# Optimization experiments

Measured on AMD Instinct MI355X. Metric: run time of the kernel, lower is better.

Reference implementation:

```python
import jax, jax.numpy as jnp
import numpy as np

NH = 12      # attention heads
EPS = 1e-5   # torch nn.LayerNorm default


def _ln(x, g, b):
    m = jnp.mean(x, axis=-1, keepdims=True)
    v = jnp.var(x, axis=-1, keepdims=True)
    return (x - m) * jax.lax.rsqrt(v + EPS) * g + b


def _rel_table(table, n):
    # q_size == k_size == n, table length == 2n-1 -> pure gather, no interpolation
    idx = jnp.arange(n)[:, None] - jnp.arange(n)[None, :] + (n - 1)
    return table[idx]  # (n, n, head_dim)


def _attn2d(x, qkv_w, qkv_b, proj_w, proj_b, rel_h, rel_w):
    B, H, W, C = x.shape
    hd = C // NH
    scale = hd ** -0.5
    N = H * W
    qkv = x.reshape(B, N, C) @ qkv_w + qkv_b                    # (B, N, 3C)
    qkv = qkv.reshape(B, N, 3, NH, hd).transpose(2, 0, 3, 1, 4).reshape(3, B * NH, N, hd)
    q, k, v = qkv[0], qkv[1], qkv[2]
    attn = jnp.einsum('bnd,bmd->bnm', q * scale, k)             # (B*NH, N, N)
    Rh = _rel_table(rel_h, H)
    Rw = _rel_table(rel_w, W)
    rq = q.reshape(B * NH, H, W, hd)                            # unscaled q, as in torch
    bias_h = jnp.einsum('bhwc,hkc->bhwk', rq, Rh)
    bias_w = jnp.einsum('bhwc,wkc->bhwk', rq, Rw)
    attn = (attn.reshape(B * NH, H, W, H, W)
            + bias_h[:, :, :, :, None]
            + bias_w[:, :, :, None, :]).reshape(B * NH, N, N)
    attn = jax.nn.softmax(attn, axis=-1)
    out = (attn @ v).reshape(B, NH, H, W, hd).transpose(0, 2, 3, 1, 4).reshape(B, H, W, C)
    return out @ proj_w + proj_b


def _win_part(x, ws):
    B, H, W, C = x.shape
    ph = (ws - H % ws) % ws
    pw = (ws - W % ws) % ws
    x = jnp.pad(x, ((0, 0), (0, ph), (0, pw), (0, 0)))
    Hp, Wp = H + ph, W + pw
    x = x.reshape(B, Hp // ws, ws, Wp // ws, ws, C).transpose(0, 1, 3, 2, 4, 5)
    return x.reshape(-1, ws, ws, C), (Hp, Wp)


def _win_unpart(wins, ws, pad_hw, hw):
    Hp, Wp = pad_hw
    H, W = hw
    B = wins.shape[0] // (Hp * Wp // ws // ws)
    x = wins.reshape(B, Hp // ws, Wp // ws, ws, ws, -1).transpose(0, 1, 3, 2, 4, 5)
    x = x.reshape(B, Hp, Wp, -1)
    return x[:, :H, :W, :]


def _block(x, ws, ln1g, ln1b, qkvw, qkvb, projw, projb, relh, relw,
           ln2g, ln2b, mw1, mb1, mw2, mb2):
    shortcut = x
    x = _ln(x, ln1g, ln1b)
    if ws > 0:
        H, W = x.shape[1], x.shape[2]
        x, pad_hw = _win_part(x, ws)
    x = _attn2d(x, qkvw, qkvb, projw, projb, relh, relw)
    if ws > 0:
        x = _win_unpart(x, ws, pad_hw, (H, W))
    x = shortcut + x
    h = _ln(x, ln2g, ln2b)
    h = jax.nn.gelu(h @ mw1 + mb1, approximate=False) @ mw2 + mb2
    return x + h


def setup_inputs() -> dict:
    key = jax.random.key(0)
    def rnd(i, shape, s=0.02):
        return jax.random.normal(jax.random.fold_in(key, i), shape, jnp.float32) * s
    C, M, HD = 768, 3072, 64
    d = {
        'x': rnd(0, (1, 3, 1024, 1024), 1.0),
        'patch_w': rnd(1, (16, 16, 3, C)),
        'patch_b': rnd(2, (C,)),
        'pos_embed': rnd(3, (1, 64, 64, C)),
    }
    i = 4
    for s, L in (('1', 27), ('2', 127)):
        for name, shape in (('ln1g', (C,)), ('ln1b', (C,)), ('qkvw', (C, 3 * C)),
                            ('qkvb', (3 * C,)), ('projw', (C, C)), ('projb', (C,)),
                            ('relh', (L, HD)), ('relw', (L, HD)),
                            ('ln2g', (C,)), ('ln2b', (C,)),
                            ('mw1', (C, M)), ('mb1', (M,)), ('mw2', (M, C)), ('mb2', (C,))):
            d[name + s] = rnd(i, shape)
            i += 1
    for s in ('1', '2'):
        d['ln1g' + s] = d['ln1g' + s] + 1.0
        d['ln2g' + s] = d['ln2g' + s] + 1.0
    return d


def reference(x, patch_w, patch_b, pos_embed,
              ln1g1, ln1b1, qkvw1, qkvb1, projw1, projb1, relh1, relw1,
              ln2g1, ln2b1, mw11, mb11, mw21, mb21,
              ln1g2, ln1b2, qkvw2, qkvb2, projw2, projb2, relh2, relw2,
              ln2g2, ln2b2, mw12, mb12, mw22, mb22):
    # patch embed: 16x16 stride-16 conv, output NHWC (B, 64, 64, 768)
    feat = jax.lax.conv_general_dilated(
        x, patch_w, window_strides=(16, 16), padding='VALID',
        dimension_numbers=('NCHW', 'HWIO', 'NHWC'))
    feat = feat + patch_b + pos_embed
    feat = _block(feat, 14, ln1g1, ln1b1, qkvw1, qkvb1, projw1, projb1,
                  relh1, relw1, ln2g1, ln2b1, mw11, mb11, mw21, mb21)
    feat = _block(feat, 0, ln1g2, ln1b2, qkvw2, qkvb2, projw2, projb2,
                  relh2, relw2, ln2g2, ln2b2, mw12, mb12, mw22, mb22)
    return feat
```

## Files before the change

kernel.cpp:

```cpp
#include <hip/hip_runtime.h>


using u16 = unsigned short;
using u32 = unsigned int;
using short8  = __attribute__((ext_vector_type(8))) short;
using floatx4 = __attribute__((ext_vector_type(4))) float;

__device__ __forceinline__ float bfu2f(u16 u) { return __builtin_bit_cast(float, (u32)u << 16); }
__device__ __forceinline__ u16   f2bfu(float f) {
  u32 u = __builtin_bit_cast(u32, f);
  return (u16)((u + 0x7fffu + ((u >> 16) & 1u)) >> 16);
}
#define DIV14(x) (((x) * 4682) >> 16)
#define WAIT_VM0()   __builtin_amdgcn_s_waitcnt(0x3f70)
#define WAIT_LGKM0() __builtin_amdgcn_s_waitcnt(0xc07f)

__device__ __forceinline__ void gld_lds16(const u16* g, u16* l) {
  __builtin_amdgcn_global_load_lds(
      (const __attribute__((address_space(1))) u32*)g,
      (__attribute__((address_space(3))) u32*)l, 16, 0, 0);
}

__global__ __launch_bounds__(256) void detect_k(const u16* __restrict__ x, int* __restrict__ flag)
{
  __shared__ int tot;
  if (threadIdx.x == 0) tot = 0;
  __syncthreads();
  int cnt = 0;
  for (int i = threadIdx.x; i < 4096; i += 256) {
    int e = (x[2 * i] >> 7) & 0xFF;
    cnt += (e >= 100 && e <= 134) ? 1 : 0;
  }
  atomicAdd(&tot, cnt);
  __syncthreads();
  if (threadIdx.x == 0) *flag = (tot >= 2458) ? 1 : 0;
}

struct CvtEnt { const void* src; int n; int dstoff; };
struct CvtArgs { CvtEnt e[24]; int cnt; };

__global__ __launch_bounds__(256) void tobf_multi_k(CvtArgs a, u16* __restrict__ dst,
                                                    const int* __restrict__ flag)
{
  int gid = blockIdx.x * 256 + threadIdx.x;
  bool isbf = (*flag != 0);
  for (int t = 0; t < a.cnt; ++t)
    if (gid < a.e[t].n)
      dst[a.e[t].dstoff + gid] = isbf ? ((const u16*)a.e[t].src)[gid]
                                      : f2bfu(((const float*)a.e[t].src)[gid]);
}

__global__ __launch_bounds__(256) void tobf4_k(const void* __restrict__ src, u16* __restrict__ dst,
                                               int n4, const int* __restrict__ flag)
{
  int i = blockIdx.x * 256 + threadIdx.x;
  if (i >= n4) return;
  ushort4 o;
  if (*flag) o = ((const ushort4*)src)[i];
  else {
    float4 f = ((const float4*)src)[i];
    o.x = f2bfu(f.x); o.y = f2bfu(f.y); o.z = f2bfu(f.z); o.w = f2bfu(f.w);
  }
  ((ushort4*)dst)[i] = o;
}

__global__ __launch_bounds__(256) void tobfT_k(const void* __restrict__ src, u16* __restrict__ dst,
                                               int K, int N, const int* __restrict__ flag)
{
  __shared__ u16 t[64][65];
  const int n0 = blockIdx.x * 64, k0 = blockIdx.y * 64;
  const int r = threadIdx.x >> 2, c = (threadIdx.x & 3) * 16;
  if (*flag) {
    const u16* s = (const u16*)src + (size_t)(k0 + r) * N + n0 + c;
    union { uint4 v[2]; u16 e[16]; } u;
    u.v[0] = *(const uint4*)s; u.v[1] = *(const uint4*)(s + 8);
    #pragma unroll
    for (int j = 0; j < 16; ++j) t[c + j][r] = u.e[j];
  } else {
    const float* s = (const float*)src + (size_t)(k0 + r) * N + n0 + c;
    #pragma unroll
    for (int j = 0; j < 16; ++j) t[c + j][r] = f2bfu(s[j]);
  }
  __syncthreads();
  union { uint4 v[2]; u16 e[16]; } o;
  #pragma unroll
  for (int j = 0; j < 16; ++j) o.e[j] = t[r][c + j];
  u16* d = dst + (size_t)(n0 + r) * K + k0 + c;
  *(uint4*)d = o.v[0]; *(uint4*)(d + 8) = o.v[1];
}

__global__ __launch_bounds__(256) void im2col_k(const void* __restrict__ xv, u16* __restrict__ a,
                                                const int* __restrict__ flag)
{
  int t = blockIdx.x, tid = threadIdx.x;
  int py = t >> 6, px = t & 63;
  int ky = tid >> 4, kx = tid & 15;
  size_t src = (size_t)(py * 16 + ky) * 1024 + px * 16 + kx;
  u16 v0, v1, v2;
  if (*flag) {
    const u16* x = (const u16*)xv;
    v0 = x[src]; v1 = x[src + 1048576]; v2 = x[src + 2097152];
  } else {
    const float* x = (const float*)xv;
    v0 = f2bfu(x[src]); v1 = f2bfu(x[src + 1048576]); v2 = f2bfu(x[src + 2097152]);
  }
  size_t dst = (size_t)t * 768 + tid * 3;
  a[dst] = v0; a[dst + 1] = v1; a[dst + 2] = v2;
}

__global__ __launch_bounds__(256) void ln_k(const float* __restrict__ x,
                                            const u16* __restrict__ g,
                                            const u16* __restrict__ b,
                                            u16* __restrict__ y)
{
  const int t = blockIdx.x, tid = threadIdx.x;
  const float* xp = x + (size_t)t * 768;
  float v0 = xp[tid], v1 = xp[tid + 256], v2 = xp[tid + 512];
  float s = v0 + v1 + v2;
  float q = v0 * v0 + v1 * v1 + v2 * v2;
  #pragma unroll
  for (int off = 32; off; off >>= 1) { s += __shfl_xor(s, off); q += __shfl_xor(q, off); }
  __shared__ float red[8];
  int wid = tid >> 6, lane = tid & 63;
  if (lane == 0) { red[wid] = s; red[4 + wid] = q; }
  __syncthreads();
  s = red[0] + red[1] + red[2] + red[3];
  q = red[4] + red[5] + red[6] + red[7];
  float mean = s * (1.f / 768.f);
  float var  = q * (1.f / 768.f) - mean * mean;
  float rstd = rsqrtf(var + 1e-5f);
  u16* yp = y + (size_t)t * 768;
  yp[tid]       = f2bfu((v0 - mean) * rstd * bfu2f(g[tid])       + bfu2f(b[tid]));
  yp[tid + 256] = f2bfu((v1 - mean) * rstd * bfu2f(g[tid + 256]) + bfu2f(b[tid + 256]));
  yp[tid + 512] = f2bfu((v2 - mean) * rstd * bfu2f(g[tid + 512]) + bfu2f(b[tid + 512]));
}

__global__ __launch_bounds__(256) void win_part_k(const u16* __restrict__ ln, u16* __restrict__ w)
{
  int vid = blockIdx.x * 256 + threadIdx.x;
  if (vid >= 470400) return;
  size_t idx = (size_t)vid * 8;
  int c = (int)(idx % 768);
  int r = (int)(idx / 768);
  int win = r / 196, tok = r - win * 196;
  int gy = (win / 5) * 14 + tok / 14;
  int gx = (win % 5) * 14 + tok % 14;
  uint4 v = make_uint4(0, 0, 0, 0);
  if (gy < 64 && gx < 64)
    v = *(const uint4*)(ln + ((size_t)(gy * 64 + gx) * 768 + c));
  *(uint4*)(w + idx) = v;
}

enum { MODE_FEAT = 0, MODE_QKV = 1, MODE_RES = 2, MODE_GELU = 3, MODE_OUT = 4 };

template<int BN>
__global__ __launch_bounds__(256) void mgemm_k(
    const u16* __restrict__ A, const u16* __restrict__ Bt, const u16* __restrict__ bias,
    int M, int N, int K, int mode,
    float* __restrict__ outf, u16* __restrict__ outb,
    const float* __restrict__ res, const u16* __restrict__ pos,
    u16* __restrict__ qb, u16* __restrict__ kb, u16* __restrict__ vt, int TW,
    const int* __restrict__ flagp)
{
  constexpr int NWN = BN / 64, NWM = 4 / NWN;
  constexpr int WTM = 128 / NWM;
  constexpr int MS = WTM / 16, NS = 4;
  __shared__ __align__(16) u16 As[2][128 * 32];
  __shared__ __align__(16) u16 Bs[2][BN * 32];
  const int tid = threadIdx.x;
  const int wid = tid >> 6, lane = tid & 63;
  const int l15 = lane & 15, quad = lane >> 4;
  const int wm = wid / NWN, wn = wid % NWN;
  const int m0 = blockIdx.y * 128, n0 = blockIdx.x * BN;

  floatx4 acc[MS][NS];
  #pragma unroll
  for (int i = 0; i < MS; ++i)
    #pragma unroll
    for (int j = 0; j < NS; ++j) acc[i][j] = (floatx4){0.f, 0.f, 0.f, 0.f};

  const int sr = lane >> 2, sc = (lane & 3) * 8;
  const u16* ag0 = A + (size_t)min(m0 + wid * 32 + sr,      M - 1) * K + sc;
  const u16* ag1 = A + (size_t)min(m0 + wid * 32 + 16 + sr, M - 1) * K + sc;
  const u16 *bg0 = nullptr, *bg1 = nullptr;
  if constexpr (BN == 128) {
    bg0 = Bt + (size_t)(n0 + wid * 32 + sr) * K + sc;
    bg1 = Bt + (size_t)(n0 + wid * 32 + 16 + sr) * K + sc;
  } else {
    bg0 = Bt + (size_t)(n0 + wid * 16 + sr) * K + sc;
  }

  auto issue = [&](int buf, int k0) {
    gld_lds16(ag0 + k0, &As[buf][(wid * 32) * 32]);
    gld_lds16(ag1 + k0, &As[buf][(wid * 32 + 16) * 32]);
    if constexpr (BN == 128) {
      gld_lds16(bg0 + k0, &Bs[buf][(wid * 32) * 32]);
      gld_lds16(bg1 + k0, &Bs[buf][(wid * 32 + 16) * 32]);
    } else {
      gld_lds16(bg0 + k0, &Bs[buf][(wid * 16) * 32]);
    }
  };

  issue(0, 0);
  int bufi = 0;
  for (int k0 = 0; k0 < K; k0 += 32, bufi ^= 1) {
    WAIT_VM0();
    __syncthreads();
    if (k0 + 32 < K) issue(bufi ^ 1, k0 + 32);
    short8 af[MS], bf[NS];
    #pragma unroll
    for (int ms = 0; ms < MS; ++ms)
      af[ms] = *(const short8*)&As[bufi][(wm * WTM + ms * 16 + l15) * 32 + quad * 8];
    #pragma unroll
    for (int ns = 0; ns < NS; ++ns)
      bf[ns] = *(const short8*)&Bs[bufi][(wn * 64 + ns * 16 + l15) * 32 + quad * 8];
    #pragma unroll
    for (int ms = 0; ms < MS; ++ms)
      #pragma unroll
      for (int ns = 0; ns < NS; ++ns)
        acc[ms][ns] = __builtin_amdgcn_mfma_f32_16x16x32_bf16(af[ms], bf[ns], acc[ms][ns], 0, 0, 0);
  }

  const bool outbf = (mode == MODE_OUT) ? (*flagp != 0) : false;
  #pragma unroll
  for (int ms = 0; ms < MS; ++ms) {
    const int gmb = m0 + wm * WTM + ms * 16 + quad * 4;
    #pragma unroll
    for (int ns = 0; ns < NS; ++ns) {
      const int gn = n0 + wn * 64 + ns * 16 + l15;
      const float bb = bfu2f(bias[gn]);
      if (mode == MODE_QKV) {
        const int s = gn / 768, nn = gn - s * 768, h = nn >> 6, d = nn & 63;
        #pragma unroll
        for (int r = 0; r < 4; ++r) {
          int gm = gmb + r; if (gm >= M) continue;
          float v = acc[ms][ns][r] + bb;
          int b = gm / TW, tok = gm - b * TW;
          size_t bh = (size_t)(b * 12 + h);
          if (s == 0)      qb[(bh * TW + tok) * 64 + d] = f2bfu(v);
          else if (s == 1) kb[(bh * TW + tok) * 64 + d] = f2bfu(v);
          else             vt[(bh * 64 + d) * TW + tok] = f2bfu(v);
        }
      } else {
        #pragma unroll
        for (int r = 0; r < 4; ++r) {
          int gm = gmb + r; if (gm >= M) continue;
          size_t o = (size_t)gm * N + gn;
          float v = acc[ms][ns][r] + bb;
          if (mode == MODE_FEAT)      outf[o] = v + bfu2f(pos[o]);
          else if (mode == MODE_RES)  outf[o] = v + res[o];
          else if (mode == MODE_GELU) outb[o] = f2bfu(0.5f * v * (1.f + erff(v * 0.70710678f)));
          else {
            float ov = v + res[o];
            if (outbf) outb[o] = f2bfu(ov);
            else       outf[o] = ov;
          }
        }
      }
    }
  }
}

template<int NT, int TD, bool WIN>
__global__ __launch_bounds__(256) void flash_k(
    const u16* __restrict__ qb, const u16* __restrict__ kb, const u16* __restrict__ vt,
    const u16* __restrict__ relh, const u16* __restrict__ relw,
    u16* __restrict__ outb)
{
  constexpr int NTAB = 2 * TD - 1;
  constexpr int KT = (NT + 63) >> 6;
  constexpr float L2E = 1.4426950408889634f;
  constexpr float SC2 = 0.125f * L2E;
  constexpr int RQ  = 0;
  constexpr int RK0 = 4096;
  constexpr int RK1 = WIN ? 4096 : 8192;
  constexpr int RV0 = WIN ? 8192 : 12288;
  constexpr int RV1 = WIN ? 8192 : 16384;
  constexpr int RG  = WIN ? 12288 : 20480;
  constexpr int GWWIN = RG + 64 * 34;
  constexpr int TOT = WIN ? (GWWIN + 64 * 34) : (RG + 64 * 66);
  __shared__ __align__(16) u16 lds[TOT];

  const int tid = threadIdx.x, wid = tid >> 6, lane = tid & 63;
  const int l15 = lane & 15, quad = lane >> 4;
  const int qt = blockIdx.x, bh = blockIdx.y;
  const int q0 = qt * 64;
  const size_t kvbase = (size_t)bh * NT * 64;
  const size_t vbase  = (size_t)bh * 64 * NT;

  auto swb = [](int row, int blk) { return row * 64 + (((blk ^ row) & 7) << 3); };

  {
    const int r = tid >> 2, cb = (tid & 3) * 2;
    const int tok = min(q0 + r, NT - 1);
    const uint4* p = (const uint4*)(qb + kvbase + (size_t)tok * 64 + cb * 8);
    *(uint4*)&lds[RQ + swb(r, cb)]     = p[0];
    *(uint4*)&lds[RQ + swb(r, cb + 1)] = p[1];
  }
  __syncthreads();
  short8 qf[2];
  qf[0] = *(const short8*)&lds[RQ + swb(wid * 16 + l15, quad)];
  qf[1] = *(const short8*)&lds[RQ + swb(wid * 16 + l15, 4 + quad)];
  WAIT_LGKM0();

  auto stageRB = [&](const u16* tab, int rowoff, int maxrow) {
    const int r = tid >> 2, cb = (tid & 3) * 2;
    const int tr = min(rowoff + r, maxrow);
    const uint4* p = (const uint4*)(tab + (size_t)tr * 64 + cb * 8);
    *(uint4*)&lds[RV0 + swb(r, cb)]     = p[0];
    *(uint4*)&lds[RV0 + swb(r, cb + 1)] = p[1];
  };
  auto gpass = [&](int gbase, int gstride, int ncols) {
    for (int ns = 0; ns < ncols / 16; ++ns) {
      floatx4 g = (floatx4){0.f, 0.f, 0.f, 0.f};
      #pragma unroll
      for (int ks = 0; ks < 2; ++ks) {
        short8 b = *(const short8*)&lds[RV0 + swb(ns * 16 + l15, ks * 4 + quad)];
        g = __builtin_amdgcn_mfma_f32_16x16x32_bf16(qf[ks], b, g, 0, 0, 0);
      }
      #pragma unroll
      for (int r = 0; r < 4; ++r)
        lds[gbase + (wid * 16 + quad * 4 + r) * gstride + ns * 16 + l15] = f2bfu(g[r] * L2E);
    }
  };

  float gwv[4][4];
  if constexpr (!WIN) {
    stageRB(relh, qt, NTAB - 1);  __syncthreads();
    gpass(RG, 66, 64);
    __syncthreads();
    stageRB(relw, 0, NTAB - 1);   __syncthreads();
    gpass(RK0, 66, 64);
    #pragma unroll
    for (int r = 0; r < 4; ++r) {
      const int tr = wid * 16 + quad * 4 + r;
      #pragma unroll
      for (int ns = 0; ns < 4; ++ns) {
        const int iw = tr - (ns * 16 + l15) + 63;
        if (iw < 64) gwv[ns][r] = bfu2f(lds[RK0 + tr * 66 + iw]);
      }
    }
    WAIT_LGKM0();
    __syncthreads();
    stageRB(relw, 64, NTAB - 1);  __syncthreads();
    gpass(RK0, 66, 64);
    #pragma unroll
    for (int r = 0; r < 4; ++r) {
      const int tr = wid * 16 + quad * 4 + r;
      #pragma unroll
      for (int ns = 0; ns < 4; ++ns) {
        const int iw = tr - (ns * 16 + l15) + 63;
        if (iw >= 64) gwv[ns][r] = bfu2f(lds[RK0 + tr * 66 + iw - 64]);
      }
    }
    WAIT_LGKM0();
  } else {
    stageRB(relh, 0, NTAB - 1);  __syncthreads();
    gpass(RG, 34, 32);
    __syncthreads();
    stageRB(relw, 0, NTAB - 1);  __syncthreads();
    gpass(GWWIN, 34, 32);
  }

  const int srow = lane >> 3;
  const int scol = (((lane & 7) ^ srow) & 7) << 3;
  const u16* kg = kb + kvbase + (size_t)(wid * 16 + srow) * 64 + scol;
  const u16* vg = vt + vbase  + (size_t)(wid * 16 + srow) * NT + scol;
  auto issue = [&](int buf, int kt2) {
    const u16* k0 = kg + (size_t)kt2 * 4096;
    const u16* v0 = vg + kt2 * 64;
    u16* kd = &lds[(buf ? RK1 : RK0) + wid * 16 * 64];
    u16* vd = &lds[(buf ? RV1 : RV0) + wid * 16 * 64];
    gld_lds16(k0,           kd);
    gld_lds16(k0 + 512,     kd + 512);
    gld_lds16(v0,           vd);
    gld_lds16(v0 + 8 * NT,  vd + 512);
  };

  float mI[4], lI[4];
  floatx4 Oacc[4];
  #pragma unroll
  for (int r = 0; r < 4; ++r) { mI[r] = -3e38f; lI[r] = 0.f; }
  #pragma unroll
  for (int d = 0; d < 4; ++d) Oacc[d] = (floatx4){0.f, 0.f, 0.f, 0.f};

  if constexpr (!WIN) { __syncthreads(); issue(0, 0); }

  for (int kt = 0; kt < KT; ++kt) {
    int RKb, RVb;
    if constexpr (!WIN) {
      WAIT_VM0();
      __syncthreads();
      if (kt + 1 < KT) issue((kt + 1) & 1, kt + 1);
      RKb = (kt & 1) ? RK1 : RK0;
      RVb = (kt & 1) ? RV1 : RV0;
    } else {
      __syncthreads();
      {
        const int r = tid >> 2, cb = (tid & 3) * 2;
        const int key = min(kt * 64 + r, NT - 1);
        const uint4* p = (const uint4*)(kb + kvbase + (size_t)key * 64 + cb * 8);
        *(uint4*)&lds[RK0 + swb(r, cb)]     = p[0];
        *(uint4*)&lds[RK0 + swb(r, cb + 1)] = p[1];
      }
      {
        const int d = tid >> 2, c = (tid & 3) << 4;
        #pragma unroll
        for (int j = 0; j < 16; ++j) {
          int key = min(kt * 64 + c + j, NT - 1);
          const int col = c + j;
          lds[RV0 + d * 64 + (((((col >> 3)) ^ d) & 7) << 3) + (col & 7)] =
              vt[vbase + (size_t)d * NT + key];
        }
      }
      __syncthreads();
      RKb = RK0; RVb = RV0;
    }

    floatx4 sacc[4];
    #pragma unroll
    for (int ns = 0; ns < 4; ++ns) sacc[ns] = (floatx4){0.f, 0.f, 0.f, 0.f};
    #pragma unroll
    for (int ks = 0; ks < 2; ++ks)
      #pragma unroll
      for (int ns = 0; ns < 4; ++ns) {
        short8 b = *(const short8*)&lds[RKb + swb(ns * 16 + l15, ks * 4 + quad)];
        sacc[ns] = __builtin_amdgcn_mfma_f32_16x16x32_bf16(qf[ks], b, sacc[ns], 0, 0, 0);
      }

    float sv[4][4];
    #pragma unroll
    for (int r = 0; r < 4; ++r) {
      if constexpr (!WIN) {
        #pragma unroll
        for (int ns = 0; ns < 4; ++ns)
          sv[ns][r] = fmaf(SC2, sacc[ns][r], gwv[ns][r]);
      } else {
        const int tr = wid * 16 + quad * 4 + r;
        const int tok = q0 + tr;
        const int qy = DIV14(tok), qx = tok - 14 * qy;
        #pragma unroll
        for (int ns = 0; ns < 4; ++ns) {
          const int j = kt * 64 + ns * 16 + l15;
          const int ky = DIV14(j), kx = j - 14 * ky;
          int ih = qy - ky + 13; ih = max(0, min(ih, 31));
          int iw = qx - kx + 13; iw = max(0, min(iw, 31));
          float s = SC2 * sacc[ns][r] + bfu2f(lds[RG + tr * 34 + ih])
                                      + bfu2f(lds[GWWIN + tr * 34 + iw]);
          sv[ns][r] = (j < NT) ? s : -1e30f;
        }
      }
    }

    #pragma unroll
    for (int r = 0; r < 4; ++r) {
      const int tr = wid * 16 + quad * 4 + r;
      float rm = fmaxf(fmaxf(sv[0][r], sv[1][r]), fmaxf(sv[2][r], sv[3][r]));
      #pragma unroll
      for (int off = 1; off < 16; off <<= 1) rm = fmaxf(rm, __shfl_xor(rm, off));
      float ghv = 0.f;
      if constexpr (!WIN) ghv = bfu2f(lds[RG + tr * 66 + (63 - kt)]);
      const float mt = rm + ghv;
      const float mn = fmaxf(mI[r], mt);
      const float al = __builtin_amdgcn_exp2f(mI[r] - mn);
      mI[r] = mn;
      const float t = mn - ghv;
      float rs = 0.f;
      #pragma unroll
      for (int ns = 0; ns < 4; ++ns) {
        float p = __builtin_amdgcn_exp2f(sv[ns][r] - t);
        rs += p;
        const int col = ns * 16 + l15;
        lds[RQ + tr * 64 + ((((col >> 3) ^ tr) & 7) << 3) + (col & 7)] = f2bfu(p);
      }
      #pragma unroll
      for (int off = 1; off < 16; off <<= 1) rs += __shfl_xor(rs, off);
      lI[r] = lI[r] * al + rs;
      #pragma unroll
      for (int d = 0; d < 4; ++d) Oacc[d][r] *= al;
    }

    #pragma unroll
    for (int ks = 0; ks < 2; ++ks) {
      short8 a = *(const short8*)&lds[RQ + swb(wid * 16 + l15, ks * 4 + quad)];
      #pragma unroll
      for (int d = 0; d < 4; ++d) {
        short8 b = *(const short8*)&lds[RVb + swb(d * 16 + l15, ks * 4 + quad)];
        Oacc[d] = __builtin_amdgcn_mfma_f32_16x16x32_bf16(a, b, Oacc[d], 0, 0, 0);
      }
    }
  }

  #pragma unroll
  for (int r = 0; r < 4; ++r) {
    const int tr = wid * 16 + quad * 4 + r;
    const float rinv = 1.f / lI[r];
    const int tok = q0 + tr;
    if constexpr (WIN) {
      if (tok >= NT) continue;
      const int win = bh / 12, h = bh - win * 12;
      const int ty = DIV14(tok), tx = tok - 14 * ty;
      const int gy = (win / 5) * 14 + ty, gx = (win % 5) * 14 + tx;
      if (gy >= 64 || gx >= 64) continue;
      u16* op = outb + (size_t)(gy * 64 + gx) * 768 + h * 64;
      #pragma unroll
      for (int d = 0; d < 4; ++d) op[d * 16 + l15] = f2bfu(Oacc[d][r] * rinv);
    } else {
      u16* op = outb + (size_t)tok * 768 + bh * 64;
      #pragma unroll
      for (int d = 0; d < 4; ++d) op[d * 16 + l15] = f2bfu(Oacc[d][r] * rinv);
    }
  }
}

extern "C" void kernel_launch(void* const* d_in, const int* in_sizes, int n_in,
                              void* d_out, int out_size, void* d_ws, size_t ws_size,
                              hipStream_t stream)
{
  const void* x      = d_in[0];
  const void* patchw = d_in[1];
  const void* patchb = d_in[2];
  const void* pos    = d_in[3];
  const void *ln1g1 = d_in[4],  *ln1b1 = d_in[5];
  const void *qkvw1 = d_in[6],  *qkvb1 = d_in[7];
  const void *projw1= d_in[8],  *projb1= d_in[9];
  const void *relh1 = d_in[10], *relw1 = d_in[11];
  const void *ln2g1 = d_in[12], *ln2b1 = d_in[13];
  const void *mw11  = d_in[14], *mb11  = d_in[15];
  const void *mw21  = d_in[16], *mb21  = d_in[17];
  const void *ln1g2 = d_in[18], *ln1b2 = d_in[19];
  const void *qkvw2 = d_in[20], *qkvb2 = d_in[21];
  const void *projw2= d_in[22], *projb2= d_in[23];
  const void *relh2 = d_in[24], *relw2 = d_in[25];
  const void *ln2g2 = d_in[26], *ln2b2 = d_in[27];
  const void *mw12  = d_in[28], *mb12  = d_in[29];
  const void *mw22  = d_in[30], *mb22  = d_in[31];

  char* w = (char*)d_ws;
  int*   FLAG = (int*)w;  w += 64;
  float* R0 = (float*)w;  w += 12582912;
  float* R1 = (float*)w;  w += 12582912;
  u16*   B0 = (u16*)w;    w += 6291456;
  u16*   Wb = (u16*)w;    w += 7526400;
  u16*   QB = (u16*)w;    w += 7526400;
  u16*   KB = (u16*)w;    w += 7526400;
  u16*   VT = (u16*)w;    w += 7526400;
  u16*   Hb = (u16*)w;    w += 25165824;
  u16*   WA = (u16*)w;    w += 14155776;
  u16*   POSb = (u16*)w;  w += 6291456;
  u16*   PRM = (u16*)w;   w += 106560;
  u16*   Ap = Hb;

  constexpr int WA_QKV = 0, WA_PROJ = 1769472, WA_M1 = 2359296, WA_M2 = 4718592;
  constexpr int PRM_PATCHB = 0, PB1 = 768, PBLK = 26240, PB2 = 768 + PBLK;
  constexpr int O_QKVB = 0, O_PROJB = 2304, O_MB1 = 3072, O_MB2 = 6144,
                O_LN1G = 6912, O_LN1B = 7680, O_LN2G = 8448, O_LN2B = 9216,
                O_RELH = 9984, O_RELW = 18112;

  detect_k<<<1, 256, 0, stream>>>((const u16*)x, FLAG);
  CvtArgs ca; int kk = 0;
  auto add = [&](const void* s, int n, int off) { ca.e[kk].src = s; ca.e[kk].n = n; ca.e[kk].dstoff = off; ++kk; };
  add(patchb, 768, PRM_PATCHB);
  add(qkvb1, 2304, PB1 + O_QKVB); add(projb1, 768, PB1 + O_PROJB);
  add(mb11, 3072, PB1 + O_MB1);   add(mb21, 768, PB1 + O_MB2);
  add(ln1g1, 768, PB1 + O_LN1G);  add(ln1b1, 768, PB1 + O_LN1B);
  add(ln2g1, 768, PB1 + O_LN2G);  add(ln2b1, 768, PB1 + O_LN2B);
  add(relh1, 27 * 64, PB1 + O_RELH); add(relw1, 27 * 64, PB1 + O_RELW);
  add(qkvb2, 2304, PB2 + O_QKVB); add(projb2, 768, PB2 + O_PROJB);
  add(mb12, 3072, PB2 + O_MB1);   add(mb22, 768, PB2 + O_MB2);
  add(ln1g2, 768, PB2 + O_LN1G);  add(ln1b2, 768, PB2 + O_LN1B);
  add(ln2g2, 768, PB2 + O_LN2G);  add(ln2b2, 768, PB2 + O_LN2B);
  add(relh2, 127 * 64, PB2 + O_RELH); add(relw2, 127 * 64, PB2 + O_RELW);
  ca.cnt = kk;
  tobf_multi_k<<<32, 256, 0, stream>>>(ca, PRM, FLAG);
  tobf4_k<<<3072, 256, 0, stream>>>(pos, POSb, 786432, FLAG);

  tobfT_k<<<dim3(12, 12), 256, 0, stream>>>(patchw, WA + WA_M1, 768, 768, FLAG);
  im2col_k<<<4096, 256, 0, stream>>>(x, Ap, FLAG);
  mgemm_k<64><<<dim3(12, 32), 256, 0, stream>>>(Ap, WA + WA_M1, PRM + PRM_PATCHB,
      4096, 768, 768, MODE_FEAT, R0, nullptr, nullptr, POSb, nullptr, nullptr, nullptr, 0, FLAG);

  tobfT_k<<<dim3(36, 12), 256, 0, stream>>>(qkvw1, WA + WA_QKV, 768, 2304, FLAG);
  tobfT_k<<<dim3(12, 12), 256, 0, stream>>>(projw1, WA + WA_PROJ, 768, 768, FLAG);
  tobfT_k<<<dim3(48, 12), 256, 0, stream>>>(mw11, WA + WA_M1, 768, 3072, FLAG);
  tobfT_k<<<dim3(12, 48), 256, 0, stream>>>(mw21, WA + WA_M2, 3072, 768, FLAG);

  ln_k<<<4096, 256, 0, stream>>>(R0, PRM + PB1 + O_LN1G, PRM + PB1 + O_LN1B, B0);
  win_part_k<<<1838, 256, 0, stream>>>(B0, Wb);
  mgemm_k<128><<<dim3(18, 39), 256, 0, stream>>>(Wb, WA + WA_QKV, PRM + PB1 + O_QKVB,
      4900, 2304, 768, MODE_QKV, nullptr, nullptr, nullptr, nullptr, QB, KB, VT, 196, FLAG);
  flash_k<196, 14, true><<<dim3(4, 300), 256, 0, stream>>>(QB, KB, VT,
      PRM + PB1 + O_RELH, PRM + PB1 + O_RELW, B0);
  mgemm_k<64><<<dim3(12, 32), 256, 0, stream>>>(B0, WA + WA_PROJ, PRM + PB1 + O_PROJB,
      4096, 768, 768, MODE_RES, R1, nullptr, R0, nullptr, nullptr, nullptr, nullptr, 0, FLAG);
  ln_k<<<4096, 256, 0, stream>>>(R1, PRM + PB1 + O_LN2G, PRM + PB1 + O_LN2B, B0);
  mgemm_k<128><<<dim3(24, 32), 256, 0, stream>>>(B0, WA + WA_M1, PRM + PB1 + O_MB1,
      4096, 3072, 768, MODE_GELU, nullptr, Hb, nullptr, nullptr, nullptr, nullptr, nullptr, 0, FLAG);
  mgemm_k<64><<<dim3(12, 32), 256, 0, stream>>>(Hb, WA + WA_M2, PRM + PB1 + O_MB2,
      4096, 768, 3072, MODE_RES, R0, nullptr, R1, nullptr, nullptr, nullptr, nullptr, 0, FLAG);

  tobfT_k<<<dim3(36, 12), 256, 0, stream>>>(qkvw2, WA + WA_QKV, 768, 2304, FLAG);
  tobfT_k<<<dim3(12, 12), 256, 0, stream>>>(projw2, WA + WA_PROJ, 768, 768, FLAG);
  tobfT_k<<<dim3(48, 12), 256, 0, stream>>>(mw12, WA + WA_M1, 768, 3072, FLAG);
  tobfT_k<<<dim3(12, 48), 256, 0, stream>>>(mw22, WA + WA_M2, 3072, 768, FLAG);

  ln_k<<<4096, 256, 0, stream>>>(R0, PRM + PB2 + O_LN1G, PRM + PB2 + O_LN1B, B0);
  mgemm_k<128><<<dim3(18, 32), 256, 0, stream>>>(B0, WA + WA_QKV, PRM + PB2 + O_QKVB,
      4096, 2304, 768, MODE_QKV, nullptr, nullptr, nullptr, nullptr, QB, KB, VT, 4096, FLAG);
  flash_k<4096, 64, false><<<dim3(64, 12), 256, 0, stream>>>(QB, KB, VT,
      PRM + PB2 + O_RELH, PRM + PB2 + O_RELW, B0);
  mgemm_k<64><<<dim3(12, 32), 256, 0, stream>>>(B0, WA + WA_PROJ, PRM + PB2 + O_PROJB,
      4096, 768, 768, MODE_RES, R1, nullptr, R0, nullptr, nullptr, nullptr, nullptr, 0, FLAG);
  ln_k<<<4096, 256, 0, stream>>>(R1, PRM + PB2 + O_LN2G, PRM + PB2 + O_LN2B, B0);
  mgemm_k<128><<<dim3(24, 32), 256, 0, stream>>>(B0, WA + WA_M1, PRM + PB2 + O_MB1,
      4096, 3072, 768, MODE_GELU, nullptr, Hb, nullptr, nullptr, nullptr, nullptr, nullptr, 0, FLAG);
  mgemm_k<64><<<dim3(12, 32), 256, 0, stream>>>(Hb, WA + WA_M2, PRM + PB2 + O_MB2,
      4096, 768, 3072, MODE_OUT, (float*)d_out, (u16*)d_out, R1, nullptr, nullptr, nullptr, nullptr, 0, FLAG);
}
```

Measured before the change: 868.4 us.

## Transpose attention MFMA so each lane owns one query row, simplifying softmax

```diff
diff --git a/kernel.cpp b/kernel.cpp
--- a/kernel.cpp
+++ b/kernel.cpp
@@ -10,6 +10,9 @@
 __device__ __forceinline__ u16   f2bfu(float f) {
   u32 u = __builtin_bit_cast(u32, f);
   return (u16)((u + 0x7fffu + ((u >> 16) & 1u)) >> 16);
+}
+__device__ __forceinline__ u32 cvtpk_bf16(float a, float b) {
+  u32 r; asm("v_cvt_pk_bf16_f32 %0, %1, %2" : "=v"(r) : "v"(a), "v"(b)); return r;
 }
 #define DIV14(x) (((x) * 4682) >> 16)
 #define WAIT_VM0()   __builtin_amdgcn_s_waitcnt(0x3f70)
@@ -287,6 +290,7 @@
   const int q0 = qt * 64;
   const size_t kvbase = (size_t)bh * NT * 64;
   const size_t vbase  = (size_t)bh * 64 * NT;
+  const int myrow = wid * 16 + l15;
 
   auto swb = [](int row, int blk) { return row * 64 + (((blk ^ row) & 7) << 3); };
 
@@ -299,8 +303,8 @@
   }
   __syncthreads();
   short8 qf[2];
-  qf[0] = *(const short8*)&lds[RQ + swb(wid * 16 + l15, quad)];
-  qf[1] = *(const short8*)&lds[RQ + swb(wid * 16 + l15, 4 + quad)];
+  qf[0] = *(const short8*)&lds[RQ + swb(myrow, quad)];
+  qf[1] = *(const short8*)&lds[RQ + swb(myrow, 4 + quad)];
   WAIT_LGKM0();
 
   auto stageRB = [&](const u16* tab, int rowoff, int maxrow) {
@@ -332,27 +336,23 @@
     stageRB(relw, 0, NTAB - 1);   __syncthreads();
     gpass(RK0, 66, 64);
     #pragma unroll
-    for (int r = 0; r < 4; ++r) {
-      const int tr = wid * 16 + quad * 4 + r;
-      #pragma unroll
-      for (int ns = 0; ns < 4; ++ns) {
-        const int iw = tr - (ns * 16 + l15) + 63;
-        if (iw < 64) gwv[ns][r] = bfu2f(lds[RK0 + tr * 66 + iw]);
-      }
-    }
+    for (int kbi = 0; kbi < 4; ++kbi)
+      #pragma unroll
+      for (int r = 0; r < 4; ++r) {
+        const int iw = myrow + 63 - (kbi * 16 + quad * 4 + r);
+        if (iw < 64) gwv[kbi][r] = bfu2f(lds[RK0 + myrow * 66 + iw]);
+      }
     WAIT_LGKM0();
     __syncthreads();
     stageRB(relw, 64, NTAB - 1);  __syncthreads();
     gpass(RK0, 66, 64);
     #pragma unroll
-    for (int r = 0; r < 4; ++r) {
-      const int tr = wid * 16 + quad * 4 + r;
-      #pragma unroll
-      for (int ns = 0; ns < 4; ++ns) {
-        const int iw = tr - (ns * 16 + l15) + 63;
-        if (iw >= 64) gwv[ns][r] = bfu2f(lds[RK0 + tr * 66 + iw - 64]);
-      }
-    }
+    for (int kbi = 0; kbi < 4; ++kbi)
+      #pragma unroll
+      for (int r = 0; r < 4; ++r) {
+        const int iw = myrow + 63 - (kbi * 16 + quad * 4 + r);
+        if (iw >= 64) gwv[kbi][r] = bfu2f(lds[RK0 + myrow * 66 + iw - 64]);
+      }
     WAIT_LGKM0();
   } else {
     stageRB(relh, 0, NTAB - 1);  __syncthreads();
@@ -377,12 +377,16 @@
     gld_lds16(v0 + 8 * NT,  vd + 512);
   };
 
-  float mI[4], lI[4];
+  float mI = -3e38f, lI = 0.f;
   floatx4 Oacc[4];
   #pragma unroll
-  for (int r = 0; r < 4; ++r) { mI[r] = -3e38f; lI[r] = 0.f; }
-  #pragma unroll
   for (int d = 0; d < 4; ++d) Oacc[d] = (floatx4){0.f, 0.f, 0.f, 0.f};
+
+  int qy = 0, qx = 0;
+  if constexpr (WIN) {
+    const int tok0 = q0 + myrow;
+    qy = DIV14(tok0); qx = tok0 - 14 * qy;
+  }
 
   if constexpr (!WIN) { __syncthreads(); issue(0, 0); }
 
@@ -405,12 +409,21 @@
       }
       {
         const int d = tid >> 2, c = (tid & 3) << 4;
-        #pragma unroll
-        for (int j = 0; j < 16; ++j) {
-          int key = min(kt * 64 + c + j, NT - 1);
-          const int col = c + j;
-          lds[RV0 + d * 64 + (((((col >> 3)) ^ d) & 7) << 3) + (col & 7)] =
-              vt[vbase + (size_t)d * NT + key];
+        if (kt * 64 + c + 15 < NT) {
+          #pragma unroll
+          for (int h = 0; h < 4; ++h) {
+            uint2 v = *(const uint2*)(vt + vbase + (size_t)d * NT + kt * 64 + c + h * 4);
+            const int col = c + h * 4;
+            *(uint2*)&lds[RV0 + d * 64 + ((((col >> 3) ^ d) & 7) << 3) + (col & 7)] = v;
+          }
+        } else {
+          #pragma unroll
+          for (int j = 0; j < 16; ++j) {
+            int key = min(kt * 64 + c + j, NT - 1);
+            const int col = c + j;
+            lds[RV0 + d * 64 + ((((col >> 3) ^ d) & 7) << 3) + (col & 7)] =
+                vt[vbase + (size_t)d * NT + key];
+          }
         }
       }
       __syncthreads();
@@ -419,97 +432,125 @@
 
     floatx4 sacc[4];
     #pragma unroll
-    for (int ns = 0; ns < 4; ++ns) sacc[ns] = (floatx4){0.f, 0.f, 0.f, 0.f};
+    for (int kbi = 0; kbi < 4; ++kbi) sacc[kbi] = (floatx4){0.f, 0.f, 0.f, 0.f};
+    __builtin_amdgcn_s_setprio(1);
     #pragma unroll
     for (int ks = 0; ks < 2; ++ks)
       #pragma unroll
-      for (int ns = 0; ns < 4; ++ns) {
-        short8 b = *(const short8*)&lds[RKb + swb(ns * 16 + l15, ks * 4 + quad)];
-        sacc[ns] = __builtin_amdgcn_mfma_f32_16x16x32_bf16(qf[ks], b, sacc[ns], 0, 0, 0);
-      }
+      for (int kbi = 0; kbi < 4; ++kbi) {
+        short8 a = *(const short8*)&lds[RKb + swb(kbi * 16 + l15, ks * 4 + quad)];
+        sacc[kbi] = __builtin_amdgcn_mfma_f32_16x16x32_bf16(a, qf[ks], sacc[kbi], 0, 0, 0);
+      }
+    __builtin_amdgcn_s_setprio(0);
 
     float sv[4][4];
-    #pragma unroll
-    for (int r = 0; r < 4; ++r) {
-      if constexpr (!WIN) {
+    if constexpr (!WIN) {
+      #pragma unroll
+      for (int kbi = 0; kbi < 4; ++kbi)
         #pragma unroll
-        for (int ns = 0; ns < 4; ++ns)
-          sv[ns][r] = fmaf(SC2, sacc[ns][r], gwv[ns][r]);
-      } else {
-        const int tr = wid * 16 + quad * 4 + r;
-        const int tok = q0 + tr;
-        const int qy = DIV14(tok), qx = tok - 14 * qy;
+        for (int r = 0; r < 4; ++r)
+          sv[kbi][r] = fmaf(SC2, sacc[kbi][r], gwv[kbi][r]);
+    } else {
+      #pragma unroll
+      for (int kbi = 0; kbi < 4; ++kbi)
         #pragma unroll
-        for (int ns = 0; ns < 4; ++ns) {
-          const int j = kt * 64 + ns * 16 + l15;
+        for (int r = 0; r < 4; ++r) {
+          const int j = kt * 64 + kbi * 16 + quad * 4 + r;
           const int ky = DIV14(j), kx = j - 14 * ky;
           int ih = qy - ky + 13; ih = max(0, min(ih, 31));
           int iw = qx - kx + 13; iw = max(0, min(iw, 31));
-          float s = SC2 * sacc[ns][r] + bfu2f(lds[RG + tr * 34 + ih])
-                                      + bfu2f(lds[GWWIN + tr * 34 + iw]);
-          sv[ns][r] = (j < NT) ? s : -1e30f;
+          float s = SC2 * sacc[kbi][r] + bfu2f(lds[RG + myrow * 34 + ih])
+                                       + bfu2f(lds[GWWIN + myrow * 34 + iw]);
+          sv[kbi][r] = (j < NT) ? s : -1e30f;
         }
-      }
-    }
-
-    #pragma unroll
-    for (int r = 0; r < 4; ++r) {
-      const int tr = wid * 16 + quad * 4 + r;
-      float rm = fmaxf(fmaxf(sv[0][r], sv[1][r]), fmaxf(sv[2][r], sv[3][r]));
-      #pragma unroll
-      for (int off = 1; off < 16; off <<= 1) rm = fmaxf(rm, __shfl_xor(rm, off));
-      float ghv = 0.f;
-      if constexpr (!WIN) ghv = bfu2f(lds[RG + tr * 66 + (63 - kt)]);
-      const float mt = rm + ghv;
-      const float mn = fmaxf(mI[r], mt);
-      const float al = __builtin_amdgcn_exp2f(mI[r] - mn);
-      mI[r] = mn;
-      const float t = mn - ghv;
-      float rs = 0.f;
-      #pragma unroll
-      for (int ns = 0; ns < 4; ++ns) {
-        float p = __builtin_amdgcn_exp2f(sv[ns][r] - t);
-        rs += p;
-        const int col = ns * 16 + l15;
-        lds[RQ + tr * 64 + ((((col >> 3) ^ tr) & 7) << 3) + (col & 7)] = f2bfu(p);
-      }
-      #pragma unroll
-      for (int off = 1; off < 16; off <<= 1) rs += __shfl_xor(rs, off);
-      lI[r] = lI[r] * al + rs;
-      #pragma unroll
-      for (int d = 0; d < 4; ++d) Oacc[d][r] *= al;
-    }
-
+    }
+
+    float rm;
+    {
+      float a0 = fmaxf(fmaxf(sv[0][0], sv[0][1]), fmaxf(sv[0][2], sv[0][3]));
+      float a1 = fmaxf(fmaxf(sv[1][0], sv[1][1]), fmaxf(sv[1][2], sv[1][3]));
+      float a2 = fmaxf(fmaxf(sv[2][0], sv[2][1]), fmaxf(sv[2][2], sv[2][3]));
+      float a3 = fmaxf(fmaxf(sv[3][0], sv[3][1]), fmaxf(sv[3][2], sv[3][3]));
+      rm = fmaxf(fmaxf(a0, a1), fmaxf(a2, a3));
+    }
+    rm = fmaxf(rm, __shfl_xor(rm, 16));
+    rm = fmaxf(rm, __shfl_xor(rm, 32));
+    float ghv = 0.f;
+    if constexpr (!WIN) ghv = bfu2f(lds[RG + myrow * 66 + (63 - kt)]);
+    const float mt = rm + ghv;
+    const float mn = fmaxf(mI, mt);
+    const float t = mn - ghv;
+
+    float rs = 0.f;
+    u32 pk[8];
+    #pragma unroll
+    for (int kbi = 0; kbi < 4; ++kbi) {
+      float p0 = __builtin_amdgcn_exp2f(sv[kbi][0] - t);
+      float p1 = __builtin_amdgcn_exp2f(sv[kbi][1] - t);
+      float p2 = __builtin_amdgcn_exp2f(sv[kbi][2] - t);
+      float p3 = __builtin_amdgcn_exp2f(sv[kbi][3] - t);
+      rs += (p0 + p1) + (p2 + p3);
+      pk[2 * kbi]     = cvtpk_bf16(p0, p1);
+      pk[2 * kbi + 1] = cvtpk_bf16(p2, p3);
+    }
+    rs += __shfl_xor(rs, 16);
+    rs += __shfl_xor(rs, 32);
+
+    #pragma unroll
+    for (int kbi = 0; kbi < 4; ++kbi) {
+      const int col = kbi * 16 + quad * 4;
+      uint2 w2; w2.x = pk[2 * kbi]; w2.y = pk[2 * kbi + 1];
+      *(uint2*)&lds[RQ + myrow * 64 + ((((col >> 3) ^ myrow) & 7) << 3) + (col & 7)] = w2;
+    }
+
+    if (__any(mt > mI)) {
+      const float al = __builtin_amdgcn_exp2f(mI - mn);
+      mI = mn;
+      lI = fmaf(lI, al, rs);
+      #pragma unroll
+      for (int d = 0; d < 4; ++d) Oacc[d] *= al;
+    } else {
+      lI += rs;
+    }
+
+    __builtin_amdgcn_s_setprio(1);
     #pragma unroll
     for (int ks = 0; ks < 2; ++ks) {
-      short8 a = *(const short8*)&lds[RQ + swb(wid * 16 + l15, ks * 4 + quad)];
+      short8 pb = *(const short8*)&lds[RQ + swb(myrow, ks * 4 + quad)];
       #pragma unroll
       for (int d = 0; d < 4; ++d) {
-        short8 b = *(const short8*)&lds[RVb + swb(d * 16 + l15, ks * 4 + quad)];
-        Oacc[d] = __builtin_amdgcn_mfma_f32_16x16x32_bf16(a, b, Oacc[d], 0, 0, 0);
-      }
-    }
-  }
-
+        short8 a = *(const short8*)&lds[RVb + swb(d * 16 + l15, ks * 4 + quad)];
+        Oacc[d] = __builtin_amdgcn_mfma_f32_16x16x32_bf16(a, pb, Oacc[d], 0, 0, 0);
+      }
+    }
+    __builtin_amdgcn_s_setprio(0);
+  }
+
+  const float rinv = 1.f / lI;
+  const int tok = q0 + myrow;
+  u32 ow[8];
   #pragma unroll
-  for (int r = 0; r < 4; ++r) {
-    const int tr = wid * 16 + quad * 4 + r;
-    const float rinv = 1.f / lI[r];
-    const int tok = q0 + tr;
-    if constexpr (WIN) {
-      if (tok >= NT) continue;
+  for (int d = 0; d < 4; ++d) {
+    ow[2 * d]     = cvtpk_bf16(Oacc[d][0] * rinv, Oacc[d][1] * rinv);
+    ow[2 * d + 1] = cvtpk_bf16(Oacc[d][2] * rinv, Oacc[d][3] * rinv);
+  }
+  if constexpr (WIN) {
+    if (tok < NT) {
       const int win = bh / 12, h = bh - win * 12;
       const int ty = DIV14(tok), tx = tok - 14 * ty;
       const int gy = (win / 5) * 14 + ty, gx = (win % 5) * 14 + tx;
-      if (gy >= 64 || gx >= 64) continue;
-      u16* op = outb + (size_t)(gy * 64 + gx) * 768 + h * 64;
-      #pragma unroll
-      for (int d = 0; d < 4; ++d) op[d * 16 + l15] = f2bfu(Oacc[d][r] * rinv);
-    } else {
-      u16* op = outb + (size_t)tok * 768 + bh * 64;
-      #pragma unroll
-      for (int d = 0; d < 4; ++d) op[d * 16 + l15] = f2bfu(Oacc[d][r] * rinv);
-    }
+      if (gy < 64 && gx < 64) {
+        u16* op = outb + (size_t)(gy * 64 + gx) * 768 + h * 64;
+        #pragma unroll
+        for (int d = 0; d < 4; ++d)
+          *(uint2*)(op + d * 16 + quad * 4) = make_uint2(ow[2 * d], ow[2 * d + 1]);
+      }
+    }
+  } else {
+    u16* op = outb + (size_t)tok * 768 + bh * 64;
+    #pragma unroll
+    for (int d = 0; d < 4; ++d)
+      *(uint2*)(op + d * 16 + quad * 4) = make_uint2(ow[2 * d], ow[2 * d + 1]);
   }
 }
 
```

Result: faster. 796.6 us (-8.3%).
